# Kernel optimization log

Measured on AMD Instinct MI355X. Metric: run time of the kernel, lower is better.

## Reference

```python
import jax, jax.numpy as jnp
import numpy as np

N, F, V, E = 16384, 39, 100000, 16
H1, H2 = 400, 400
EPS = 1e-5

def setup_inputs() -> dict:
    key = jax.random.key(0)
    ks = jax.random.split(key, 12)
    xi = jax.random.randint(ks[0], (N, F, 1), 0, V)  # indices per field
    xv = jax.random.uniform(ks[1], (N, F), dtype=jnp.float32)
    # stacked per-field embedding tables (each table has V+1 rows)
    emb1 = jax.random.normal(ks[2], (F, V + 1), dtype=jnp.float32)          # 1st-order
    emb2 = jax.random.normal(ks[3], (F, V + 1, E), dtype=jnp.float32)       # 2nd-order
    D = F * E
    W1 = jax.random.normal(ks[4], (D, H1), dtype=jnp.float32) / np.sqrt(D)
    b1 = jnp.zeros((H1,), jnp.float32)
    g1 = jnp.ones((H1,), jnp.float32)
    be1 = jnp.zeros((H1,), jnp.float32)
    W2 = jax.random.normal(ks[5], (H1, H2), dtype=jnp.float32) / np.sqrt(H1)
    b2 = jnp.zeros((H2,), jnp.float32)
    g2 = jnp.ones((H2,), jnp.float32)
    be2 = jnp.zeros((H2,), jnp.float32)
    bias = jax.random.normal(ks[6], (1,), dtype=jnp.float32)
    return dict(xi=xi, xv=xv, emb1=emb1, emb2=emb2, W1=W1, b1=b1, g1=g1, be1=be1,
                W2=W2, b2=b2, g2=g2, be2=be2, bias=bias)

def _batchnorm(x, g, b):
    # BatchNorm1d in training mode: batch mean/var (biased)
    mu = x.mean(0)
    var = x.var(0)
    return g * (x - mu) * jax.lax.rsqrt(var + EPS) + b

def reference(xi, xv, emb1, emb2, W1, b1, g1, be1, W2, b2, g2, be2, bias):
    idx = xi[:, :, 0]                     # (N, F)
    f_ids = jnp.arange(F)[None, :]        # (1, F)
    e1 = emb1[f_ids, idx] * xv            # (N, F): per-field 1st-order term
    e2 = emb2[f_ids, idx] * xv[:, :, None]  # (N, F, E)
    s = e2.sum(axis=1)                    # (N, E) sum of embeddings
    fm2 = 0.5 * (s * s - (e2 * e2).sum(axis=1))  # (N, E) FM 2nd-order
    deep = e2.reshape(e2.shape[0], F * E)
    h = _batchnorm(deep @ W1 + b1, g1, be1)       # dropout = identity (eval)
    h = _batchnorm(h @ W2 + b2, g2, be2)
    return e1.sum(axis=1) + fm2.sum(axis=1) + h.sum(axis=1) + bias[0]
```

## Files before the change

kernel.cpp:

```cpp
#include <hip/hip_runtime.h>
#include <hip/hip_bf16.h>

#define Nn 16384
#define Ff 39
#define Vv 100000
#define Ee 16
#define Dd 624
#define Hh 400
#define EPSf 1e-5f

typedef short short8 __attribute__((ext_vector_type(8)));
typedef float floatx4 __attribute__((ext_vector_type(4)));

__device__ __forceinline__ float bf2f(unsigned short v) {
  union { unsigned int u; float f; } x; x.u = ((unsigned int)v) << 16; return x.f;
}

__global__ __launch_bounds__(256) void embed_kernel(
    const int* __restrict__ xi, const float* __restrict__ xv,
    const float* __restrict__ emb1, const float* __restrict__ emb2,
    const float* __restrict__ bias, const float* __restrict__ W1,
    __hip_bfloat16* __restrict__ deep, float* __restrict__ p,
    __hip_bfloat16* __restrict__ W1t, float* __restrict__ stats) {
  const int b = blockIdx.x;
  if (b >= 4096) {
    if (b == 4496) {
      for (int i = threadIdx.x; i < 1600; i += 256) stats[i] = 0.f;
    } else {
      const int n = b - 4096;
      for (int k = threadIdx.x; k < Dd; k += 256)
        W1t[(size_t)n * Dd + k] = __float2bfloat16(W1[(size_t)k * Hh + n]);
    }
    return;
  }
  __shared__ int   sidx[4][40];
  __shared__ float sxv[4][40];
  const int w = threadIdx.x >> 6;
  const int lane = threadIdx.x & 63;
  const int n = b * 4 + w;
  if (lane < Ff) {
    sidx[w][lane] = xi[n * Ff + lane];
    sxv[w][lane]  = xv[n * Ff + lane];
  }
  __syncthreads();

  float s_e = 0.f, sq_e = 0.f;
  #pragma unroll
  for (int j = lane; j < Dd; j += 64) {
    const int f = j >> 4;
    const long off = ((long)f * (Vv + 1) + sidx[w][f]) * Ee + (j & 15);
    const float v = emb2[off] * sxv[w][f];
    deep[(long)n * Dd + j] = __float2bfloat16(v);
    s_e += v; sq_e += v * v;
  }
  s_e  += __shfl_xor(s_e, 16);  sq_e += __shfl_xor(sq_e, 16);
  s_e  += __shfl_xor(s_e, 32);  sq_e += __shfl_xor(sq_e, 32);

  float val = (lane < Ee) ? 0.5f * (s_e * s_e - sq_e) : 0.f;
  if (lane < Ff)
    val += emb1[(long)lane * (Vv + 1) + sidx[w][lane]] * sxv[w][lane];
  #pragma unroll
  for (int d = 1; d < 64; d <<= 1) val += __shfl_xor(val, d);
  if (lane == 0) p[n] = val + bias[0];
}

__global__ __launch_bounds__(256) void gemm_bf16(
    const __hip_bfloat16* __restrict__ A, const __hip_bfloat16* __restrict__ Wt,
    const float* __restrict__ bias, __hip_bfloat16* __restrict__ C,
    float* __restrict__ s, float* __restrict__ ss, int K) {
  __shared__ uint4 As4[128 * 9];
  __shared__ uint4 Bs4[80 * 9];
  const int tid = threadIdx.x;
  const int n0 = blockIdx.x * 80;
  const int m0 = blockIdx.y * 128;
  const int w = tid >> 6, lane = tid & 63;
  const int lm = lane & 15, qd = lane >> 4;

  floatx4 acc[2][5];
  #pragma unroll
  for (int i = 0; i < 2; ++i)
    #pragma unroll
    for (int j = 0; j < 5; ++j)
      acc[i][j] = (floatx4){0.f, 0.f, 0.f, 0.f};

  const short* As_s = (const short*)As4;
  const short* Bs_s = (const short*)Bs4;
  const int nk = (K + 63) >> 6;

  for (int ks = 0; ks < nk; ++ks) {
    const int k0 = ks << 6;
    #pragma unroll
    for (int cc = 0; cc < 4; ++cc) {
      const int c = tid + cc * 256;
      const int m = c >> 3, kc = c & 7;
      const int k = k0 + kc * 8;
      uint4 v = make_uint4(0, 0, 0, 0);
      if (k < K) v = *(const uint4*)&A[(size_t)(m0 + m) * K + k];
      As4[m * 9 + kc] = v;
    }
    for (int c = tid; c < 640; c += 256) {
      const int n = c >> 3, kc = c & 7;
      const int k = k0 + kc * 8;
      uint4 v = make_uint4(0, 0, 0, 0);
      if (k < K) v = *(const uint4*)&Wt[(size_t)(n0 + n) * K + k];
      Bs4[n * 9 + kc] = v;
    }
    __syncthreads();
    #pragma unroll
    for (int h = 0; h < 2; ++h) {
      const int ko = h * 32 + qd * 8;
      const short8 a0 = *(const short8*)&As_s[(w * 32 + 0  + lm) * 72 + ko];
      const short8 a1 = *(const short8*)&As_s[(w * 32 + 16 + lm) * 72 + ko];
      #pragma unroll
      for (int nt = 0; nt < 5; ++nt) {
        const short8 b = *(const short8*)&Bs_s[(nt * 16 + lm) * 72 + ko];
        acc[0][nt] = __builtin_amdgcn_mfma_f32_16x16x32_bf16(a0, b, acc[0][nt], 0, 0, 0);
        acc[1][nt] = __builtin_amdgcn_mfma_f32_16x16x32_bf16(a1, b, acc[1][nt], 0, 0, 0);
      }
    }
    __syncthreads();
  }

  const int rb = m0 + w * 32 + qd * 4;
  #pragma unroll
  for (int nt = 0; nt < 5; ++nt) {
    const int col = n0 + nt * 16 + lm;
    const float bc = bias[col];
    float cs = 0.f, cq = 0.f;
    #pragma unroll
    for (int mt = 0; mt < 2; ++mt) {
      #pragma unroll
      for (int r = 0; r < 4; ++r) {
        const float v = acc[mt][nt][r] + bc;
        const __hip_bfloat16 hv = __float2bfloat16(v);
        C[(size_t)(rb + mt * 16 + r) * Hh + col] = hv;
        const float vf = __bfloat162float(hv);
        cs += vf; cq += vf * vf;
      }
    }
    cs += __shfl_xor(cs, 16); cq += __shfl_xor(cq, 16);
    cs += __shfl_xor(cs, 32); cq += __shfl_xor(cq, 32);
    if (lane < 16) { atomicAdd(&s[col], cs); atomicAdd(&ss[col], cq); }
  }
}

__global__ __launch_bounds__(256) void prep2_kernel(
    const float* __restrict__ W2,
    const float* __restrict__ s1, const float* __restrict__ ss1,
    const float* __restrict__ g1, const float* __restrict__ be1,
    const float* __restrict__ b2, __hip_bfloat16* __restrict__ W2t, float* __restrict__ b2p) {
  __shared__ float sa1[Hh], sc1[Hh];
  __shared__ float red[256];
  const int n = blockIdx.x, t = threadIdx.x;
  for (int k = t; k < Hh; k += 256) {
    const float mu = s1[k] * (1.f / Nn);
    const float var = ss1[k] * (1.f / Nn) - mu * mu;
    const float a = g1[k] * rsqrtf(var + EPSf);
    sa1[k] = a;
    sc1[k] = be1[k] - a * mu;
  }
  __syncthreads();
  float acc = 0.f;
  for (int k = t; k < Hh; k += 256) {
    const float wv = W2[(size_t)k * Hh + n];
    W2t[(size_t)n * Hh + k] = __float2bfloat16(sa1[k] * wv);
    acc += sc1[k] * wv;
  }
  red[t] = acc; __syncthreads();
  for (int d = 128; d > 0; d >>= 1) { if (t < d) red[t] += red[t + d]; __syncthreads(); }
  if (t == 0) b2p[n] = b2[n] + red[0];
}

__global__ __launch_bounds__(256) void final_kernel(
    const __hip_bfloat16* __restrict__ x2,
    const float* __restrict__ s2, const float* __restrict__ ss2,
    const float* __restrict__ g2, const float* __restrict__ be2,
    const float* __restrict__ p, float* __restrict__ out) {
  __shared__ float sal[Hh];
  __shared__ float red[256];
  const int t = threadIdx.x;
  float part = 0.f;
  for (int h = t; h < Hh; h += 256) {
    const float mu = s2[h] * (1.f / Nn);
    const float var = ss2[h] * (1.f / Nn) - mu * mu;
    const float al = g2[h] * rsqrtf(var + EPSf);
    sal[h] = al;
    part += be2[h] - al * mu;
  }
  red[t] = part; __syncthreads();
  for (int d = 128; d > 0; d >>= 1) { if (t < d) red[t] += red[t + d]; __syncthreads(); }
  __syncthreads();
  const float c2 = red[0];

  const int w = t >> 6, lane = t & 63;
  const int n = blockIdx.x * 4 + w;
  const unsigned short* row = (const unsigned short*)(x2 + (size_t)n * Hh);
  float acc = 0.f;
  for (int h0 = lane * 4; h0 < Hh; h0 += 256) {
    const ushort4 u = *(const ushort4*)&row[h0];
    acc += bf2f(u.x) * sal[h0] + bf2f(u.y) * sal[h0 + 1]
         + bf2f(u.z) * sal[h0 + 2] + bf2f(u.w) * sal[h0 + 3];
  }
  #pragma unroll
  for (int d = 1; d < 64; d <<= 1) acc += __shfl_xor(acc, d);
  if (lane == 0) out[n] = p[n] + acc + c2;
}

extern "C" void kernel_launch(void* const* d_in, const int* in_sizes, int n_in,
                              void* d_out, int out_size, void* d_ws, size_t ws_size,
                              hipStream_t stream) {
  const int*   xi   = (const int*)d_in[0];
  const float* xv   = (const float*)d_in[1];
  const float* emb1 = (const float*)d_in[2];
  const float* emb2 = (const float*)d_in[3];
  const float* W1   = (const float*)d_in[4];
  const float* b1   = (const float*)d_in[5];
  const float* g1   = (const float*)d_in[6];
  const float* be1  = (const float*)d_in[7];
  const float* W2   = (const float*)d_in[8];
  const float* b2   = (const float*)d_in[9];
  const float* g2   = (const float*)d_in[10];
  const float* be2  = (const float*)d_in[11];
  const float* bias = (const float*)d_in[12];
  float* out = (float*)d_out;

  char* ws = (char*)d_ws;
  __hip_bfloat16* deep = (__hip_bfloat16*)ws;  ws += (size_t)Nn * Dd * 2;
  __hip_bfloat16* x1b  = (__hip_bfloat16*)ws;  ws += (size_t)Nn * Hh * 2;
  __hip_bfloat16* x2b  = (__hip_bfloat16*)ws;  ws += (size_t)Nn * Hh * 2;
  __hip_bfloat16* W1t  = (__hip_bfloat16*)ws;  ws += (size_t)Hh * Dd * 2;
  __hip_bfloat16* W2t  = (__hip_bfloat16*)ws;  ws += (size_t)Hh * Hh * 2;
  float* p    = (float*)ws;  ws += (size_t)Nn * 4;
  float* s1   = (float*)ws;  ws += Hh * 4;
  float* ss1  = (float*)ws;  ws += Hh * 4;
  float* s2   = (float*)ws;  ws += Hh * 4;
  float* ss2  = (float*)ws;  ws += Hh * 4;
  float* b2p  = (float*)ws;  ws += Hh * 4;

  embed_kernel<<<4497, 256, 0, stream>>>(xi, xv, emb1, emb2, bias, W1, deep, p, W1t, s1);
  gemm_bf16<<<dim3(5, Nn / 128), 256, 0, stream>>>(deep, W1t, b1, x1b, s1, ss1, Dd);
  prep2_kernel<<<Hh, 256, 0, stream>>>(W2, s1, ss1, g1, be1, b2, W2t, b2p);
  gemm_bf16<<<dim3(5, Nn / 128), 256, 0, stream>>>(x1b, W2t, b2p, x2b, s2, ss2, Hh);
  final_kernel<<<Nn / 4, 256, 0, stream>>>(x2b, s2, ss2, g2, be2, p, out);
}
```

Before: 431.1 us.

## Pad GEMM K dims, use direct global-to-LDS loads with XOR swizzle, vectorize embed

Activation and weight buffers are padded to K multiples of 64 (640 and 448) so the GEMM can drop bounds checks and use global_load_lds 16-byte transfers straight into an XOR-swizzled LDS layout, which avoids register staging and bank conflicts. The block index is remapped so neighbouring blocks are spread across the grid, and the per-column BN statistics are first reduced in LDS before atomics, cutting atomic traffic by four. The embedding gather now uses float4 loads and ushort4 stores, and it zero-fills the padding columns. The cost is extra padded memory plus the zero writes, and correctness now depends on the padding being kept consistent.

Result: faster. 381.1 us (median of 2 runs) (-11.6%).

```diff
diff --git a/kernel.cpp b/kernel.cpp
--- a/kernel.cpp
+++ b/kernel.cpp
@@ -6,14 +6,26 @@
 #define Vv 100000
 #define Ee 16
 #define Dd 624
+#define KP1 640
+#define KP2 448
 #define Hh 400
 #define EPSf 1e-5f
 
 typedef short short8 __attribute__((ext_vector_type(8)));
 typedef float floatx4 __attribute__((ext_vector_type(4)));
 
+__device__ __forceinline__ unsigned short f2bu(float x) {
+  __hip_bfloat16 h = __float2bfloat16(x);
+  return *reinterpret_cast<unsigned short*>(&h);
+}
 __device__ __forceinline__ float bf2f(unsigned short v) {
   union { unsigned int u; float f; } x; x.u = ((unsigned int)v) << 16; return x.f;
+}
+
+__device__ __forceinline__ void gload16(void* lds, const void* g) {
+  __builtin_amdgcn_global_load_lds(
+      (const __attribute__((address_space(1))) unsigned int*)g,
+      (__attribute__((address_space(3))) unsigned int*)lds, 16, 0, 0);
 }
 
 __global__ __launch_bounds__(256) void embed_kernel(
@@ -21,15 +33,17 @@
     const float* __restrict__ emb1, const float* __restrict__ emb2,
     const float* __restrict__ bias, const float* __restrict__ W1,
     __hip_bfloat16* __restrict__ deep, float* __restrict__ p,
-    __hip_bfloat16* __restrict__ W1t, float* __restrict__ stats) {
+    __hip_bfloat16* __restrict__ W1t, float* __restrict__ stats,
+    __hip_bfloat16* __restrict__ x1b) {
   const int b = blockIdx.x;
   if (b >= 4096) {
     if (b == 4496) {
       for (int i = threadIdx.x; i < 1600; i += 256) stats[i] = 0.f;
     } else {
       const int n = b - 4096;
-      for (int k = threadIdx.x; k < Dd; k += 256)
-        W1t[(size_t)n * Dd + k] = __float2bfloat16(W1[(size_t)k * Hh + n]);
+      for (int k = threadIdx.x; k < KP1; k += 256)
+        W1t[(size_t)n * KP1 + k] =
+            (k < Dd) ? __float2bfloat16(W1[(size_t)k * Hh + n]) : __float2bfloat16(0.f);
     }
     return;
   }
@@ -44,19 +58,39 @@
   }
   __syncthreads();
 
-  float s_e = 0.f, sq_e = 0.f;
-  #pragma unroll
-  for (int j = lane; j < Dd; j += 64) {
-    const int f = j >> 4;
-    const long off = ((long)f * (Vv + 1) + sidx[w][f]) * Ee + (j & 15);
-    const float v = emb2[off] * sxv[w][f];
-    deep[(long)n * Dd + j] = __float2bfloat16(v);
-    s_e += v; sq_e += v * v;
-  }
-  s_e  += __shfl_xor(s_e, 16);  sq_e += __shfl_xor(sq_e, 16);
-  s_e  += __shfl_xor(s_e, 32);  sq_e += __shfl_xor(sq_e, 32);
-
-  float val = (lane < Ee) ? 0.5f * (s_e * s_e - sq_e) : 0.f;
+  const float4* e2v = (const float4*)emb2;
+  float se0 = 0.f, se1 = 0.f, se2 = 0.f, se3 = 0.f;
+  float qe0 = 0.f, qe1 = 0.f, qe2 = 0.f, qe3 = 0.f;
+  #pragma unroll
+  for (int t = 0; t < 3; ++t) {
+    const int j4 = lane + t * 64;
+    if (j4 < 156) {
+      const int f = j4 >> 2;
+      float4 v = e2v[((long)f * (Vv + 1) + sidx[w][f]) * 4 + (j4 & 3)];
+      const float xf = sxv[w][f];
+      v.x *= xf; v.y *= xf; v.z *= xf; v.w *= xf;
+      *(ushort4*)&deep[(size_t)n * KP1 + j4 * 4] =
+          make_ushort4(f2bu(v.x), f2bu(v.y), f2bu(v.z), f2bu(v.w));
+      se0 += v.x; qe0 += v.x * v.x;
+      se1 += v.y; qe1 += v.y * v.y;
+      se2 += v.z; qe2 += v.z * v.z;
+      se3 += v.w; qe3 += v.w * v.w;
+    }
+  }
+  if (lane < 4)  *(ushort4*)&deep[(size_t)n * KP1 + Dd + lane * 4] = make_ushort4(0, 0, 0, 0);
+  if (lane < 12) *(ushort4*)&x1b [(size_t)n * KP2 + Hh + lane * 4] = make_ushort4(0, 0, 0, 0);
+
+  #pragma unroll
+  for (int d = 4; d < 64; d <<= 1) {
+    se0 += __shfl_xor(se0, d); qe0 += __shfl_xor(qe0, d);
+    se1 += __shfl_xor(se1, d); qe1 += __shfl_xor(qe1, d);
+    se2 += __shfl_xor(se2, d); qe2 += __shfl_xor(qe2, d);
+    se3 += __shfl_xor(se3, d); qe3 += __shfl_xor(qe3, d);
+  }
+  float val = 0.f;
+  if (lane < 4)
+    val = 0.5f * ((se0 * se0 - qe0) + (se1 * se1 - qe1) +
+                  (se2 * se2 - qe2) + (se3 * se3 - qe3));
   if (lane < Ff)
     val += emb1[(long)lane * (Vv + 1) + sidx[w][lane]] * sxv[w][lane];
   #pragma unroll
@@ -67,12 +101,15 @@
 __global__ __launch_bounds__(256) void gemm_bf16(
     const __hip_bfloat16* __restrict__ A, const __hip_bfloat16* __restrict__ Wt,
     const float* __restrict__ bias, __hip_bfloat16* __restrict__ C,
-    float* __restrict__ s, float* __restrict__ ss, int K) {
-  __shared__ uint4 As4[128 * 9];
-  __shared__ uint4 Bs4[80 * 9];
+    float* __restrict__ s, float* __restrict__ ss, const int K, const int ldc) {
+  __shared__ __align__(16) short As_s[128 * 64];
+  __shared__ __align__(16) short Bs_s[80 * 64];
+  __shared__ float redS[4][5][16], redQ[4][5][16];
   const int tid = threadIdx.x;
-  const int n0 = blockIdx.x * 80;
-  const int m0 = blockIdx.y * 128;
+  const int lin = blockIdx.x + blockIdx.y * 5;
+  const int v   = (lin & 7) * 80 + (lin >> 3);
+  const int n0  = (v % 5) * 80;
+  const int m0  = (v / 5) * 128;
   const int w = tid >> 6, lane = tid & 63;
   const int lm = lane & 15, qd = lane >> 4;
 
@@ -83,39 +120,36 @@
     for (int j = 0; j < 5; ++j)
       acc[i][j] = (floatx4){0.f, 0.f, 0.f, 0.f};
 
-  const short* As_s = (const short*)As4;
-  const short* Bs_s = (const short*)Bs4;
-  const int nk = (K + 63) >> 6;
-
+  const int nk = K >> 6;
   for (int ks = 0; ks < nk; ++ks) {
     const int k0 = ks << 6;
     #pragma unroll
-    for (int cc = 0; cc < 4; ++cc) {
-      const int c = tid + cc * 256;
+    for (int j = 0; j < 4; ++j) {
+      const int c = tid + j * 256;
       const int m = c >> 3, kc = c & 7;
-      const int k = k0 + kc * 8;
-      uint4 v = make_uint4(0, 0, 0, 0);
-      if (k < K) v = *(const uint4*)&A[(size_t)(m0 + m) * K + k];
-      As4[m * 9 + kc] = v;
-    }
-    for (int c = tid; c < 640; c += 256) {
-      const int n = c >> 3, kc = c & 7;
-      const int k = k0 + kc * 8;
-      uint4 v = make_uint4(0, 0, 0, 0);
-      if (k < K) v = *(const uint4*)&Wt[(size_t)(n0 + n) * K + k];
-      Bs4[n * 9 + kc] = v;
+      gload16(&As_s[c * 8], &A[(size_t)(m0 + m) * K + k0 + ((kc ^ (m & 7)) << 3)]);
+    }
+    #pragma unroll
+    for (int j = 0; j < 3; ++j) {
+      const int c = tid + j * 256;
+      if (c < 640) {
+        const int nn = c >> 3, kc = c & 7;
+        gload16(&Bs_s[c * 8], &Wt[(size_t)(n0 + nn) * K + k0 + ((kc ^ (nn & 7)) << 3)]);
+      }
     }
     __syncthreads();
     #pragma unroll
     for (int h = 0; h < 2; ++h) {
-      const int ko = h * 32 + qd * 8;
-      const short8 a0 = *(const short8*)&As_s[(w * 32 + 0  + lm) * 72 + ko];
-      const short8 a1 = *(const short8*)&As_s[(w * 32 + 16 + lm) * 72 + ko];
+      const int sl = (h * 32 + qd * 8) >> 3;
+      const int r0 = w * 32 + lm, r1 = r0 + 16;
+      const short8 a0 = *(const short8*)&As_s[r0 * 64 + ((sl ^ (r0 & 7)) << 3)];
+      const short8 a1 = *(const short8*)&As_s[r1 * 64 + ((sl ^ (r1 & 7)) << 3)];
       #pragma unroll
       for (int nt = 0; nt < 5; ++nt) {
-        const short8 b = *(const short8*)&Bs_s[(nt * 16 + lm) * 72 + ko];
-        acc[0][nt] = __builtin_amdgcn_mfma_f32_16x16x32_bf16(a0, b, acc[0][nt], 0, 0, 0);
-        acc[1][nt] = __builtin_amdgcn_mfma_f32_16x16x32_bf16(a1, b, acc[1][nt], 0, 0, 0);
+        const int rn = nt * 16 + lm;
+        const short8 bfr = *(const short8*)&Bs_s[rn * 64 + ((sl ^ (rn & 7)) << 3)];
+        acc[0][nt] = __builtin_amdgcn_mfma_f32_16x16x32_bf16(a0, bfr, acc[0][nt], 0, 0, 0);
+        acc[1][nt] = __builtin_amdgcn_mfma_f32_16x16x32_bf16(a1, bfr, acc[1][nt], 0, 0, 0);
       }
     }
     __syncthreads();
@@ -131,16 +165,23 @@
     for (int mt = 0; mt < 2; ++mt) {
       #pragma unroll
       for (int r = 0; r < 4; ++r) {
-        const float v = acc[mt][nt][r] + bc;
-        const __hip_bfloat16 hv = __float2bfloat16(v);
-        C[(size_t)(rb + mt * 16 + r) * Hh + col] = hv;
+        const float vv = acc[mt][nt][r] + bc;
+        const __hip_bfloat16 hv = __float2bfloat16(vv);
+        C[(size_t)(rb + mt * 16 + r) * ldc + col] = hv;
         const float vf = __bfloat162float(hv);
         cs += vf; cq += vf * vf;
       }
     }
     cs += __shfl_xor(cs, 16); cq += __shfl_xor(cq, 16);
     cs += __shfl_xor(cs, 32); cq += __shfl_xor(cq, 32);
-    if (lane < 16) { atomicAdd(&s[col], cs); atomicAdd(&ss[col], cq); }
+    if (lane < 16) { redS[w][nt][lm] = cs; redQ[w][nt][lm] = cq; }
+  }
+  __syncthreads();
+  if (tid < 80) {
+    const int nt = tid >> 4, l = tid & 15;
+    const int col = n0 + nt * 16 + l;
+    atomicAdd(&s[col],  redS[0][nt][l] + redS[1][nt][l] + redS[2][nt][l] + redS[3][nt][l]);
+    atomicAdd(&ss[col], redQ[0][nt][l] + redQ[1][nt][l] + redQ[2][nt][l] + redQ[3][nt][l]);
   }
 }
 
@@ -161,10 +202,14 @@
   }
   __syncthreads();
   float acc = 0.f;
-  for (int k = t; k < Hh; k += 256) {
-    const float wv = W2[(size_t)k * Hh + n];
-    W2t[(size_t)n * Hh + k] = __float2bfloat16(sa1[k] * wv);
-    acc += sc1[k] * wv;
+  for (int k = t; k < KP2; k += 256) {
+    if (k < Hh) {
+      const float wv = W2[(size_t)k * Hh + n];
+      W2t[(size_t)n * KP2 + k] = __float2bfloat16(sa1[k] * wv);
+      acc += sc1[k] * wv;
+    } else {
+      W2t[(size_t)n * KP2 + k] = __float2bfloat16(0.f);
+    }
   }
   red[t] = acc; __syncthreads();
   for (int d = 128; d > 0; d >>= 1) { if (t < d) red[t] += red[t + d]; __syncthreads(); }
@@ -225,11 +270,11 @@
   float* out = (float*)d_out;
 
   char* ws = (char*)d_ws;
-  __hip_bfloat16* deep = (__hip_bfloat16*)ws;  ws += (size_t)Nn * Dd * 2;
-  __hip_bfloat16* x1b  = (__hip_bfloat16*)ws;  ws += (size_t)Nn * Hh * 2;
+  __hip_bfloat16* deep = (__hip_bfloat16*)ws;  ws += (size_t)Nn * KP1 * 2;
+  __hip_bfloat16* x1b  = (__hip_bfloat16*)ws;  ws += (size_t)Nn * KP2 * 2;
   __hip_bfloat16* x2b  = (__hip_bfloat16*)ws;  ws += (size_t)Nn * Hh * 2;
-  __hip_bfloat16* W1t  = (__hip_bfloat16*)ws;  ws += (size_t)Hh * Dd * 2;
-  __hip_bfloat16* W2t  = (__hip_bfloat16*)ws;  ws += (size_t)Hh * Hh * 2;
+  __hip_bfloat16* W1t  = (__hip_bfloat16*)ws;  ws += (size_t)Hh * KP1 * 2;
+  __hip_bfloat16* W2t  = (__hip_bfloat16*)ws;  ws += (size_t)Hh * KP2 * 2;
   float* p    = (float*)ws;  ws += (size_t)Nn * 4;
   float* s1   = (float*)ws;  ws += Hh * 4;
   float* ss1  = (float*)ws;  ws += Hh * 4;
@@ -237,9 +282,9 @@
   float* ss2  = (float*)ws;  ws += Hh * 4;
   float* b2p  = (float*)ws;  ws += Hh * 4;
 
-  embed_kernel<<<4497, 256, 0, stream>>>(xi, xv, emb1, emb2, bias, W1, deep, p, W1t, s1);
-  gemm_bf16<<<dim3(5, Nn / 128), 256, 0, stream>>>(deep, W1t, b1, x1b, s1, ss1, Dd);
+  embed_kernel<<<4497, 256, 0, stream>>>(xi, xv, emb1, emb2, bias, W1, deep, p, W1t, s1, x1b);
+  gemm_bf16<<<dim3(5, Nn / 128), 256, 0, stream>>>(deep, W1t, b1, x1b, s1, ss1, KP1, KP2);
   prep2_kernel<<<Hh, 256, 0, stream>>>(W2, s1, ss1, g1, be1, b2, W2t, b2p);
-  gemm_bf16<<<dim3(5, Nn / 128), 256, 0, stream>>>(x1b, W2t, b2p, x2b, s2, ss2, Hh);
+  gemm_bf16<<<dim3(5, Nn / 128), 256, 0, stream>>>(x1b, W2t, b2p, x2b, s2, ss2, KP2, Hh);
   final_kernel<<<Nn / 4, 256, 0, stream>>>(x2b, s2, ss2, g2, be2, p, out);
 }
```
